# Performance work log

Measured on AMD Instinct MI355X. Metric: run time of the kernel, lower is better.

## Reference

```python
import jax, jax.numpy as jnp
import numpy as np

B, S, D_MODEL, H, D_HEAD = 4, 2048, 1024, 16, 64
SCALE = D_HEAD ** -0.5


def setup_inputs() -> dict:
    key = jax.random.key(0)
    ks = jax.random.split(key, 6)
    init = lambda k, shp: jax.random.normal(k, shp, jnp.float32) * (shp[0] ** -0.5)
    Xq = jax.random.normal(ks[0], (B, S, D_MODEL), jnp.float32)
    # pre-softmax bool mask: True = masked (fill -inf) -> causal
    mask_bef = jnp.triu(jnp.ones((S, S), dtype=bool), k=1)
    # post-softmax bool mask: True = zero out that attention weight
    mask_aft = jax.random.bernoulli(ks[1], 0.1, (S, S))
    Wq = init(ks[2], (D_MODEL, H * D_HEAD))
    Wk = init(ks[3], (D_MODEL, H * D_HEAD))
    Wv = init(ks[4], (D_MODEL, H * D_HEAD))
    Wo = init(ks[5], (H * D_HEAD, D_MODEL))
    return {"Xq": Xq, "mask_bef": mask_bef, "mask_aft": mask_aft,
            "Wq": Wq, "Wk": Wk, "Wv": Wv, "Wo": Wo}


def reference(Xq, mask_bef, mask_aft, Wq, Wk, Wv, Wo):
    # Self-attention: Xk = Xv = Xq
    def split_heads(X, W):  # [B,S,D] @ [D,H*d] -> [B,H,S,d]
        return (X @ W).reshape(B, S, H, D_HEAD).transpose(0, 2, 1, 3)

    Q = split_heads(Xq, Wq)
    K = split_heads(Xq, Wk)
    V = split_heads(Xq, Wv)
    # scores: [B,H,Sq,Sk]
    scores = jnp.einsum('bhqd,bhkd->bhqk', Q, K) * SCALE
    scores = jnp.where(mask_bef, -jnp.inf, scores)  # pre-softmax bool mask
    attn = jax.nn.softmax(scores, axis=-1)
    attn = jnp.where(mask_aft, 0.0, attn)           # post-softmax bool mask
    out = jnp.einsum('bhqk,bhkd->bhqd', attn, V)    # [B,H,S,d]
    out = out.transpose(0, 2, 1, 3).reshape(B, S, H * D_HEAD)
    return out @ Wo  # [B,S,out_dim_o]
```

## Files before the change

### kernel.cpp

```cpp
#include <hip/hip_runtime.h>
#include <hip/hip_bf16.h>


using bf16 = __hip_bfloat16;
typedef __attribute__((ext_vector_type(8))) short short8;
typedef __attribute__((ext_vector_type(4))) float floatx4;

#define kB 4
#define kS 2048
#define kDM 1024
#define kH 16
#define kDH 64
#define kHeadElems ((size_t)kB * kH * kS * kDH)
#define STR 72

__device__ __forceinline__ float bfu(unsigned short v) {
    return __uint_as_float(((unsigned)v) << 16);
}
__device__ __forceinline__ unsigned short f2bf(float f) {
    union { float f; unsigned u; } x{f};
    unsigned r = x.u + 0x7fff + ((x.u >> 16) & 1);
    return (unsigned short)(r >> 16);
}
__device__ __forceinline__ void gl_lds16(const void* g, void* l) {
    __builtin_amdgcn_global_load_lds(
        (const __attribute__((address_space(1))) unsigned int*)g,
        (__attribute__((address_space(3))) unsigned int*)l, 16, 0, 0);
}

__global__ __launch_bounds__(256)
void pack_mask(const int* __restrict__ mask_aft, unsigned long long* __restrict__ mp)
{
    const int widx = blockIdx.x * 4 + (threadIdx.x >> 6);
    const int lane = threadIdx.x & 63;
    const int q = widx >> 5, w64 = widx & 31;
    const int key = w64 * 64 + lane;
    const int m = mask_aft[(size_t)q * kS + key];
    const unsigned long long b = __ballot(m != 0 || key > q);
    if (lane == 0) mp[widx] = b;
}

__global__ __launch_bounds__(256)
void conv_x(const float* __restrict__ X, bf16* __restrict__ Xb)
{
    const size_t i = ((size_t)blockIdx.x * 256 + threadIdx.x) * 8;
    const float4 a = *(const float4*)(X + i);
    const float4 b = *(const float4*)(X + i + 4);
    union { unsigned short u[8]; uint4 v; } o;
    o.u[0] = f2bf(a.x); o.u[1] = f2bf(a.y); o.u[2] = f2bf(a.z); o.u[3] = f2bf(a.w);
    o.u[4] = f2bf(b.x); o.u[5] = f2bf(b.y); o.u[6] = f2bf(b.z); o.u[7] = f2bf(b.w);
    *(uint4*)(Xb + i) = o.v;
}

__global__ __launch_bounds__(256)
void conv_wT(const float* __restrict__ W, bf16* __restrict__ WT)
{
    __shared__ unsigned short Ls[64][STR];
    const int k0 = blockIdx.x * 64, n0 = blockIdx.y * 64;
    const int tid = threadIdx.x;
    const int r16 = tid >> 4, c4 = (tid & 15) * 4;
    #pragma unroll
    for (int it = 0; it < 4; ++it) {
        const int r = it * 16 + r16;
        const float4 v = *(const float4*)(W + (size_t)(k0 + r) * kDM + n0 + c4);
        Ls[c4 + 0][r] = f2bf(v.x); Ls[c4 + 1][r] = f2bf(v.y);
        Ls[c4 + 2][r] = f2bf(v.z); Ls[c4 + 3][r] = f2bf(v.w);
    }
    __syncthreads();
    #pragma unroll
    for (int it = 0; it < 4; ++it) {
        const int rn = it * 16 + r16;
        ushort4 u;
        u.x = Ls[rn][c4 + 0]; u.y = Ls[rn][c4 + 1];
        u.z = Ls[rn][c4 + 2]; u.w = Ls[rn][c4 + 3];
        *(ushort4*)(WT + (size_t)(n0 + rn) * kDM + k0 + c4) = u;
    }
}

__global__ __launch_bounds__(256)
void qkv_mfma(const bf16* __restrict__ A, const bf16* __restrict__ BT,
              bf16* __restrict__ ws)
{
    __shared__ __align__(16) unsigned short At[128][32];
    __shared__ __align__(16) unsigned short Bt[128][32];
    const int tid = threadIdx.x;
    const int w = tid >> 6, lane = tid & 63;
    const int quad = (tid >> 4) & 3, col = tid & 15;
    const int wm = w >> 1, wn = w & 1;
    const int n0 = blockIdx.x * 128;
    const int m0 = blockIdx.y * 128;

    const bf16* pA = A  + (size_t)(m0 + w * 32 + (lane >> 2)) * kDM + (lane & 3) * 8;
    const bf16* pB = BT + (size_t)(n0 + w * 32 + (lane >> 2)) * kDM + (lane & 3) * 8;
    unsigned short* lA = &At[w * 32][0];
    unsigned short* lB = &Bt[w * 32][0];

    floatx4 acc[4][4];
    #pragma unroll
    for (int i = 0; i < 4; ++i)
        #pragma unroll
        for (int j = 0; j < 4; ++j) acc[i][j] = (floatx4){0.f, 0.f, 0.f, 0.f};

    for (int k0 = 0; k0 < kDM; k0 += 32) {
        __syncthreads();
        gl_lds16(pA + k0, lA);
        gl_lds16(pA + k0 + 16 * kDM, lA + 16 * 32);
        gl_lds16(pB + k0, lB);
        gl_lds16(pB + k0 + 16 * kDM, lB + 16 * 32);
        __syncthreads();
        short8 aA[4], bB[4];
        #pragma unroll
        for (int i = 0; i < 4; ++i)
            aA[i] = *(const short8*)&At[wm * 64 + i * 16 + col][quad * 8];
        #pragma unroll
        for (int j = 0; j < 4; ++j)
            bB[j] = *(const short8*)&Bt[wn * 64 + j * 16 + col][quad * 8];
        #pragma unroll
        for (int i = 0; i < 4; ++i)
            #pragma unroll
            for (int j = 0; j < 4; ++j)
                acc[i][j] = __builtin_amdgcn_mfma_f32_16x16x32_bf16(aA[i], bB[j], acc[i][j], 0, 0, 0);
    }

    const int p  = n0 >> 10;
    const int nn = n0 & 1023;
    const float scl = (p == 0) ? 0.125f : 1.0f;
    bf16* Out = ws + (size_t)p * kHeadElems;
    #pragma unroll
    for (int i = 0; i < 4; ++i) {
        #pragma unroll
        for (int r = 0; r < 4; ++r) {
            const int m = m0 + wm * 64 + i * 16 + quad * 4 + r;
            const int b = m >> 11, s = m & 2047;
            #pragma unroll
            for (int j = 0; j < 4; ++j) {
                const int n = nn + wn * 64 + j * 16 + col;
                const int h = n >> 6, d = n & 63;
                Out[((size_t)(b * kH + h) * kS + s) * kDH + d] = __float2bfloat16(acc[i][j][r] * scl);
            }
        }
    }
}

__global__ __launch_bounds__(256)
void vtrans(const bf16* __restrict__ V, bf16* __restrict__ VT)
{
    const int bh = blockIdx.y;
    const int s0 = blockIdx.x * 64;
    const bf16* src = V + (size_t)bh * kS * kDH;
    bf16* dst = VT + (size_t)bh * kS * kDH;
    __shared__ unsigned short L[64][STR];
    const int tid = threadIdx.x;
    #pragma unroll
    for (int t = 0; t < 2; ++t) {
        const int idx = t * 256 + tid;
        const int r = idx >> 3, c8 = (idx & 7) * 8;
        *(uint4*)&L[r][c8] = *(const uint4*)(src + (size_t)(s0 + r) * kDH + c8);
    }
    __syncthreads();
    #pragma unroll
    for (int t = 0; t < 2; ++t) {
        const int idx = t * 256 + tid;
        const int d = idx >> 3, sc = (idx & 7) * 8;
        unsigned short tmp[8];
        #pragma unroll
        for (int e = 0; e < 8; ++e) tmp[e] = L[sc + e][d];
        *(uint4*)(dst + (size_t)d * kS + s0 + sc) = *(uint4*)tmp;
    }
}

__global__ __launch_bounds__(256)
void attn_mfma(const bf16* __restrict__ ws, const bf16* __restrict__ VT,
               const unsigned long long* __restrict__ mp,
               bf16* __restrict__ Aout)
{
    const int bh = blockIdx.y;
    const int b = bh >> 4, h = bh & 15;
    const int qtile = 31 - blockIdx.x;
    const int q0 = qtile * 64;
    const int tid = threadIdx.x;
    const int w    = tid >> 6;
    const int lane = tid & 63;
    const int quad = (tid >> 4) & 3;
    const int col  = tid & 15;

    const size_t ho = (size_t)bh * kS * kDH;
    const bf16* Qg  = ws + ho;
    const bf16* Kg  = ws + kHeadElems + ho;
    const bf16* VTg = VT + ho;

    __shared__ __align__(16) unsigned short Ks[64][64];
    __shared__ __align__(16) unsigned short Vs[64][64];
    __shared__ __align__(16) unsigned short Pw[4][16][STR];
    __shared__ unsigned long long Mw[64];

    const int qw = q0 + w * 16;
    const short8 bQ0 = *(const short8*)(Qg + (size_t)(qw + col) * kDH + quad * 8);
    const short8 bQ1 = *(const short8*)(Qg + (size_t)(qw + col) * kDH + 32 + quad * 8);

    const int swz = col & 7;
    const int sch = (lane & 7) ^ (lane >> 3);

    floatx4 Ov[4] = {{0.f,0.f,0.f,0.f},{0.f,0.f,0.f,0.f},{0.f,0.f,0.f,0.f},{0.f,0.f,0.f,0.f}};
    float lacc = 0.f;

    for (int kt = 0; kt <= qtile; ++kt) {
        __syncthreads();
        #pragma unroll
        for (int t = 0; t < 2; ++t) {
            const int rbase = (t * 4 + w) * 8;
            const int r = rbase + (lane >> 3);
            gl_lds16(Kg  + (size_t)(kt * 64 + r) * kDH + sch * 8, &Ks[rbase][0]);
            gl_lds16(VTg + (size_t)r * kS + kt * 64 + sch * 8,    &Vs[rbase][0]);
        }
        if (tid < 64) Mw[tid] = mp[(size_t)(q0 + tid) * 32 + kt];
        __syncthreads();

        floatx4 sg[4];
        #pragma unroll
        for (int g = 0; g < 4; ++g) {
            const int krow = g * 16 + col;
            const short8 aK0 = *(const short8*)&Ks[krow][(quad ^ swz) * 8];
            const short8 aK1 = *(const short8*)&Ks[krow][((4 + quad) ^ swz) * 8];
            floatx4 s = {0.f, 0.f, 0.f, 0.f};
            s = __builtin_amdgcn_mfma_f32_16x16x32_bf16(aK0, bQ0, s, 0, 0, 0);
            s = __builtin_amdgcn_mfma_f32_16x16x32_bf16(aK1, bQ1, s, 0, 0, 0);
            sg[g] = s;
        }

        const unsigned long long wr = Mw[w * 16 + col] >> (quad * 4);
        const unsigned wlo = (unsigned)wr, whi = (unsigned)(wr >> 32);
        float pv[16];
        if (kt == qtile) {
            #pragma unroll
            for (int g = 0; g < 4; ++g)
                #pragma unroll
                for (int r = 0; r < 4; ++r) {
                    const int key = kt * 64 + g * 16 + quad * 4 + r;
                    const float pe = __expf(sg[g][r]);
                    const float p = (key <= qw + col) ? pe : 0.f;
                    lacc += p;
                    const unsigned wsel = (g < 2) ? wlo : whi;
                    pv[g * 4 + r] = ((wsel >> ((g & 1) * 16 + r)) & 1u) ? 0.f : p;
                }
        } else {
            #pragma unroll
            for (int g = 0; g < 4; ++g)
                #pragma unroll
                for (int r = 0; r < 4; ++r) {
                    const float p = __expf(sg[g][r]);
                    lacc += p;
                    const unsigned wsel = (g < 2) ? wlo : whi;
                    pv[g * 4 + r] = ((wsel >> ((g & 1) * 16 + r)) & 1u) ? 0.f : p;
                }
        }

        #pragma unroll
        for (int g = 0; g < 4; ++g) {
            const unsigned b0 = __float_as_uint(pv[g * 4 + 0]) + 0x8000u;
            const unsigned b1 = __float_as_uint(pv[g * 4 + 1]) + 0x8000u;
            const unsigned b2 = __float_as_uint(pv[g * 4 + 2]) + 0x8000u;
            const unsigned b3 = __float_as_uint(pv[g * 4 + 3]) + 0x8000u;
            uint2 pk;
            pk.x = __builtin_amdgcn_perm(b1, b0, 0x07060302u);
            pk.y = __builtin_amdgcn_perm(b3, b2, 0x07060302u);
            *(uint2*)&Pw[w][col][g * 16 + quad * 4] = pk;
        }

        const short8 aP0 = *(const short8*)&Pw[w][col][quad * 8];
        const short8 aP1 = *(const short8*)&Pw[w][col][32 + quad * 8];
        #pragma unroll
        for (int dg = 0; dg < 4; ++dg) {
            const int vrow = dg * 16 + col;
            const short8 bV0 = *(const short8*)&Vs[vrow][(quad ^ swz) * 8];
            const short8 bV1 = *(const short8*)&Vs[vrow][((4 + quad) ^ swz) * 8];
            Ov[dg] = __builtin_amdgcn_mfma_f32_16x16x32_bf16(aP0, bV0, Ov[dg], 0, 0, 0);
            Ov[dg] = __builtin_amdgcn_mfma_f32_16x16x32_bf16(aP1, bV1, Ov[dg], 0, 0, 0);
        }
    }

    float l = lacc;
    l += __shfl_xor(l, 16, 64);
    l += __shfl_xor(l, 32, 64);
    const float linv = 1.f / l;
    #pragma unroll
    for (int r = 0; r < 4; ++r) {
        const float sc = __shfl(linv, quad * 4 + r, 64);
        const int q = qw + quad * 4 + r;
        bf16* orow = Aout + ((size_t)(b * kS + q)) * kDM + h * kDH;
        #pragma unroll
        for (int dg = 0; dg < 4; ++dg)
            orow[dg * 16 + col] = __float2bfloat16(Ov[dg][r] * sc);
    }
}

__global__ __launch_bounds__(256)
void out_mfma(const bf16* __restrict__ A, const bf16* __restrict__ BT,
              float* __restrict__ Out)
{
    __shared__ __align__(16) unsigned short At[128][32];
    __shared__ __align__(16) unsigned short Bt[128][32];
    const int tid = threadIdx.x;
    const int w = tid >> 6, lane = tid & 63;
    const int quad = (tid >> 4) & 3, col = tid & 15;
    const int wm = w >> 1, wn = w & 1;
    const int n0 = blockIdx.x * 128;
    const int m0 = blockIdx.y * 128;

    const bf16* pA = A  + (size_t)(m0 + w * 32 + (lane >> 2)) * kDM + (lane & 3) * 8;
    const bf16* pB = BT + (size_t)(n0 + w * 32 + (lane >> 2)) * kDM + (lane & 3) * 8;
    unsigned short* lA = &At[w * 32][0];
    unsigned short* lB = &Bt[w * 32][0];

    floatx4 acc[4][4];
    #pragma unroll
    for (int i = 0; i < 4; ++i)
        #pragma unroll
        for (int j = 0; j < 4; ++j) acc[i][j] = (floatx4){0.f, 0.f, 0.f, 0.f};

    for (int k0 = 0; k0 < kDM; k0 += 32) {
        __syncthreads();
        gl_lds16(pA + k0, lA);
        gl_lds16(pA + k0 + 16 * kDM, lA + 16 * 32);
        gl_lds16(pB + k0, lB);
        gl_lds16(pB + k0 + 16 * kDM, lB + 16 * 32);
        __syncthreads();
        short8 aA[4], bB[4];
        #pragma unroll
        for (int i = 0; i < 4; ++i)
            aA[i] = *(const short8*)&At[wm * 64 + i * 16 + col][quad * 8];
        #pragma unroll
        for (int j = 0; j < 4; ++j)
            bB[j] = *(const short8*)&Bt[wn * 64 + j * 16 + col][quad * 8];
        #pragma unroll
        for (int i = 0; i < 4; ++i)
            #pragma unroll
            for (int j = 0; j < 4; ++j)
                acc[i][j] = __builtin_amdgcn_mfma_f32_16x16x32_bf16(aA[i], bB[j], acc[i][j], 0, 0, 0);
    }

    #pragma unroll
    for (int i = 0; i < 4; ++i)
        #pragma unroll
        for (int r = 0; r < 4; ++r) {
            const int m = m0 + wm * 64 + i * 16 + quad * 4 + r;
            #pragma unroll
            for (int j = 0; j < 4; ++j)
                Out[(size_t)m * kDM + n0 + wn * 64 + j * 16 + col] = acc[i][j][r];
        }
}

extern "C" void kernel_launch(void* const* d_in, const int* in_sizes, int n_in,
                              void* d_out, int out_size, void* d_ws, size_t ws_size,
                              hipStream_t stream)
{
    const float* Xq       = (const float*)d_in[0];
    const int*   mask_aft = (const int*)d_in[2];
    const float* Wq       = (const float*)d_in[3];
    const float* Wk       = (const float*)d_in[4];
    const float* Wv       = (const float*)d_in[5];
    const float* Wo       = (const float*)d_in[6];
    float* out = (float*)d_out;

    bf16* ws   = (bf16*)d_ws;
    bf16* Xbf  = ws + 3 * kHeadElems;
    bf16* Aout = Xbf;
    bf16* WoT  = ws;

    unsigned long long* mp = (unsigned long long*)d_out;
    bf16* WcatT = (bf16*)d_out + 262144;
    bf16* VT    = (bf16*)((char*)d_out + 8u * 1024 * 1024);

    pack_mask<<<dim3(kS * 32 / 4), 256, 0, stream>>>(mask_aft, mp);
    conv_x  <<<dim3(4096), 256, 0, stream>>>(Xq, Xbf);
    conv_wT <<<dim3(16, 16), 256, 0, stream>>>(Wq, WcatT);
    conv_wT <<<dim3(16, 16), 256, 0, stream>>>(Wk, WcatT + (size_t)kDM * kDM);
    conv_wT <<<dim3(16, 16), 256, 0, stream>>>(Wv, WcatT + 2 * (size_t)kDM * kDM);
    qkv_mfma<<<dim3(24, 64), 256, 0, stream>>>(Xbf, WcatT, ws);
    vtrans  <<<dim3(32, 64), 256, 0, stream>>>(ws + 2 * kHeadElems, VT);
    attn_mfma<<<dim3(32, 64), 256, 0, stream>>>(ws, VT, mp, Aout);
    conv_wT <<<dim3(16, 16), 256, 0, stream>>>(Wo, WoT);
    out_mfma<<<dim3(8, 64), 256, 0, stream>>>(Aout, WoT, out);
}
```

Measured before the change: 350.1 us.

## Restructure attention with 128-query tiles, double-buffered K/V, exp2 and row-major QKV

The attention kernel now gives each block 128 queries (32 per wave, in two 16-row groups). K/V tiles are double-buffered so the next tile's global-to-LDS load overlaps compute, and the K and V fragments are loaded once and reused for both query groups. The softmax folds log2(e) into the Q scale so it can use exp2, and the causal check runs only on diagonal tiles. QKV is written row-major instead of head-split, and the three weight conversions are merged into one launch. Risks include higher register pressure under the 3-blocks-per-CU launch bound, fewer blocks in the grid, and strided Q/K reads.

```diff
diff --git a/kernel.cpp b/kernel.cpp
--- a/kernel.cpp
+++ b/kernel.cpp
@@ -13,10 +13,8 @@
 #define kDH 64
 #define kHeadElems ((size_t)kB * kH * kS * kDH)
 #define STR 72
-
-__device__ __forceinline__ float bfu(unsigned short v) {
-    return __uint_as_float(((unsigned)v) << 16);
-}
+#define kQScale 0.1803368801f
+
 __device__ __forceinline__ unsigned short f2bf(float f) {
     union { float f; unsigned u; } x{f};
     unsigned r = x.u + 0x7fff + ((x.u >> 16) & 1);
@@ -52,8 +50,8 @@
     *(uint4*)(Xb + i) = o.v;
 }
 
-__global__ __launch_bounds__(256)
-void conv_wT(const float* __restrict__ W, bf16* __restrict__ WT)
+__device__ __forceinline__ void conv_wT_body(const float* __restrict__ W,
+                                             bf16* __restrict__ WT)
 {
     __shared__ unsigned short Ls[64][STR];
     const int k0 = blockIdx.x * 64, n0 = blockIdx.y * 64;
@@ -75,6 +73,21 @@
         u.z = Ls[rn][c4 + 2]; u.w = Ls[rn][c4 + 3];
         *(ushort4*)(WT + (size_t)(n0 + rn) * kDM + k0 + c4) = u;
     }
+}
+
+__global__ __launch_bounds__(256)
+void conv_w3(const float* __restrict__ Wq, const float* __restrict__ Wk,
+             const float* __restrict__ Wv, bf16* __restrict__ WT)
+{
+    const int z = blockIdx.z;
+    const float* W = (z == 0) ? Wq : ((z == 1) ? Wk : Wv);
+    conv_wT_body(W, WT + (size_t)z * kDM * kDM);
+}
+
+__global__ __launch_bounds__(256)
+void conv_wT(const float* __restrict__ W, bf16* __restrict__ WT)
+{
+    conv_wT_body(W, WT);
 }
 
 __global__ __launch_bounds__(256)
@@ -122,22 +135,19 @@
                 acc[i][j] = __builtin_amdgcn_mfma_f32_16x16x32_bf16(aA[i], bB[j], acc[i][j], 0, 0, 0);
     }
 
-    const int p  = n0 >> 10;
-    const int nn = n0 & 1023;
-    const float scl = (p == 0) ? 0.125f : 1.0f;
+    const int p   = n0 >> 10;
+    const int nn0 = n0 & 1023;
+    const float scl = (p == 0) ? kQScale : 1.0f;
     bf16* Out = ws + (size_t)p * kHeadElems;
     #pragma unroll
     for (int i = 0; i < 4; ++i) {
         #pragma unroll
         for (int r = 0; r < 4; ++r) {
             const int m = m0 + wm * 64 + i * 16 + quad * 4 + r;
-            const int b = m >> 11, s = m & 2047;
-            #pragma unroll
-            for (int j = 0; j < 4; ++j) {
-                const int n = nn + wn * 64 + j * 16 + col;
-                const int h = n >> 6, d = n & 63;
-                Out[((size_t)(b * kH + h) * kS + s) * kDH + d] = __float2bfloat16(acc[i][j][r] * scl);
-            }
+            bf16* base = Out + (size_t)m * kDM + nn0 + wn * 64 + col;
+            #pragma unroll
+            for (int j = 0; j < 4; ++j)
+                base[j * 16] = __float2bfloat16(acc[i][j][r] * scl);
         }
     }
 }
@@ -146,8 +156,9 @@
 void vtrans(const bf16* __restrict__ V, bf16* __restrict__ VT)
 {
     const int bh = blockIdx.y;
+    const int b = bh >> 4, h = bh & 15;
     const int s0 = blockIdx.x * 64;
-    const bf16* src = V + (size_t)bh * kS * kDH;
+    const bf16* src = V + ((size_t)b * kS) * kDM + h * kDH;
     bf16* dst = VT + (size_t)bh * kS * kDH;
     __shared__ unsigned short L[64][STR];
     const int tid = threadIdx.x;
@@ -155,7 +166,7 @@
     for (int t = 0; t < 2; ++t) {
         const int idx = t * 256 + tid;
         const int r = idx >> 3, c8 = (idx & 7) * 8;
-        *(uint4*)&L[r][c8] = *(const uint4*)(src + (size_t)(s0 + r) * kDH + c8);
+        *(uint4*)&L[r][c8] = *(const uint4*)(src + (size_t)(s0 + r) * kDM + c8);
     }
     __syncthreads();
     #pragma unroll
@@ -169,128 +180,151 @@
     }
 }
 
-__global__ __launch_bounds__(256)
-void attn_mfma(const bf16* __restrict__ ws, const bf16* __restrict__ VT,
-               const unsigned long long* __restrict__ mp,
+__global__ __launch_bounds__(256, 3)
+void attn_mfma(const bf16* __restrict__ Qb, const bf16* __restrict__ Kb,
+               const bf16* __restrict__ VT, const unsigned long long* __restrict__ mp,
                bf16* __restrict__ Aout)
 {
     const int bh = blockIdx.y;
     const int b = bh >> 4, h = bh & 15;
-    const int qtile = 31 - blockIdx.x;
-    const int q0 = qtile * 64;
+    const int qtile = 15 - blockIdx.x;
+    const int q0 = qtile * 128;
     const int tid = threadIdx.x;
     const int w    = tid >> 6;
     const int lane = tid & 63;
     const int quad = (tid >> 4) & 3;
     const int col  = tid & 15;
 
-    const size_t ho = (size_t)bh * kS * kDH;
-    const bf16* Qg  = ws + ho;
-    const bf16* Kg  = ws + kHeadElems + ho;
-    const bf16* VTg = VT + ho;
-
-    __shared__ __align__(16) unsigned short Ks[64][64];
-    __shared__ __align__(16) unsigned short Vs[64][64];
+    const bf16* Qg  = Qb + ((size_t)b * kS) * kDM + h * kDH;
+    const bf16* Kg  = Kb + ((size_t)b * kS) * kDM + h * kDH;
+    const bf16* VTg = VT + (size_t)bh * kS * kDH;
+
+    __shared__ __align__(16) unsigned short Ks[2][64][64];
+    __shared__ __align__(16) unsigned short Vs[2][64][64];
     __shared__ __align__(16) unsigned short Pw[4][16][STR];
-    __shared__ unsigned long long Mw[64];
-
-    const int qw = q0 + w * 16;
-    const short8 bQ0 = *(const short8*)(Qg + (size_t)(qw + col) * kDH + quad * 8);
-    const short8 bQ1 = *(const short8*)(Qg + (size_t)(qw + col) * kDH + 32 + quad * 8);
+    __shared__ unsigned long long Mw[2][128];
 
     const int swz = col & 7;
     const int sch = (lane & 7) ^ (lane >> 3);
 
-    floatx4 Ov[4] = {{0.f,0.f,0.f,0.f},{0.f,0.f,0.f,0.f},{0.f,0.f,0.f,0.f},{0.f,0.f,0.f,0.f}};
-    float lacc = 0.f;
-
-    for (int kt = 0; kt <= qtile; ++kt) {
-        __syncthreads();
+    short8 bQ[2][2];
+    #pragma unroll
+    for (int qg = 0; qg < 2; ++qg) {
+        const int qr = q0 + w * 32 + qg * 16 + col;
+        bQ[qg][0] = *(const short8*)(Qg + (size_t)qr * kDM + quad * 8);
+        bQ[qg][1] = *(const short8*)(Qg + (size_t)qr * kDM + 32 + quad * 8);
+    }
+
+    floatx4 Ov[2][4];
+    #pragma unroll
+    for (int qg = 0; qg < 2; ++qg)
+        #pragma unroll
+        for (int dg = 0; dg < 4; ++dg) Ov[qg][dg] = (floatx4){0.f, 0.f, 0.f, 0.f};
+    float lacc[2] = {0.f, 0.f};
+
+    const int nkt = 2 * qtile + 2;
+
+    auto stage = [&](int kt, int buf) {
         #pragma unroll
         for (int t = 0; t < 2; ++t) {
             const int rbase = (t * 4 + w) * 8;
             const int r = rbase + (lane >> 3);
-            gl_lds16(Kg  + (size_t)(kt * 64 + r) * kDH + sch * 8, &Ks[rbase][0]);
-            gl_lds16(VTg + (size_t)r * kS + kt * 64 + sch * 8,    &Vs[rbase][0]);
-        }
-        if (tid < 64) Mw[tid] = mp[(size_t)(q0 + tid) * 32 + kt];
+            gl_lds16(Kg  + (size_t)(kt * 64 + r) * kDM + sch * 8, &Ks[buf][rbase][0]);
+            gl_lds16(VTg + (size_t)r * kS + kt * 64 + sch * 8,    &Vs[buf][rbase][0]);
+        }
+        if (tid < 128) Mw[buf][tid] = mp[(size_t)(q0 + tid) * 32 + kt];
+    };
+
+    stage(0, 0);
+
+    for (int kt = 0; kt < nkt; ++kt) {
+        const int cur = kt & 1;
         __syncthreads();
-
-        floatx4 sg[4];
+        if (kt + 1 < nkt) stage(kt + 1, cur ^ 1);
+
+        if (kt * 64 > q0 + w * 32 + 31) continue;
+
+        short8 aK[4][2];
         #pragma unroll
         for (int g = 0; g < 4; ++g) {
             const int krow = g * 16 + col;
-            const short8 aK0 = *(const short8*)&Ks[krow][(quad ^ swz) * 8];
-            const short8 aK1 = *(const short8*)&Ks[krow][((4 + quad) ^ swz) * 8];
-            floatx4 s = {0.f, 0.f, 0.f, 0.f};
-            s = __builtin_amdgcn_mfma_f32_16x16x32_bf16(aK0, bQ0, s, 0, 0, 0);
-            s = __builtin_amdgcn_mfma_f32_16x16x32_bf16(aK1, bQ1, s, 0, 0, 0);
-            sg[g] = s;
-        }
-
-        const unsigned long long wr = Mw[w * 16 + col] >> (quad * 4);
-        const unsigned wlo = (unsigned)wr, whi = (unsigned)(wr >> 32);
-        float pv[16];
-        if (kt == qtile) {
-            #pragma unroll
-            for (int g = 0; g < 4; ++g)
+            aK[g][0] = *(const short8*)&Ks[cur][krow][(quad ^ swz) * 8];
+            aK[g][1] = *(const short8*)&Ks[cur][krow][((4 + quad) ^ swz) * 8];
+        }
+        short8 bV[4][2];
+        #pragma unroll
+        for (int dg = 0; dg < 4; ++dg) {
+            const int vrow = dg * 16 + col;
+            bV[dg][0] = *(const short8*)&Vs[cur][vrow][(quad ^ swz) * 8];
+            bV[dg][1] = *(const short8*)&Vs[cur][vrow][((4 + quad) ^ swz) * 8];
+        }
+
+        #pragma unroll
+        for (int qg = 0; qg < 2; ++qg) {
+            const int qw = q0 + w * 32 + qg * 16;
+            if (kt * 64 > qw + 15) continue;
+
+            floatx4 sg[4];
+            #pragma unroll
+            for (int g = 0; g < 4; ++g) {
+                floatx4 s = {0.f, 0.f, 0.f, 0.f};
+                s = __builtin_amdgcn_mfma_f32_16x16x32_bf16(aK[g][0], bQ[qg][0], s, 0, 0, 0);
+                s = __builtin_amdgcn_mfma_f32_16x16x32_bf16(aK[g][1], bQ[qg][1], s, 0, 0, 0);
+                sg[g] = s;
+            }
+
+            const unsigned long long wr = Mw[cur][w * 32 + qg * 16 + col] >> (quad * 4);
+            const unsigned wlo = (unsigned)wr, whi = (unsigned)(wr >> 32);
+            const bool diag = (kt * 64 + 63 > qw);
+
+            #pragma unroll
+            for (int g = 0; g < 4; ++g) {
+                float pv[4];
                 #pragma unroll
                 for (int r = 0; r < 4; ++r) {
-                    const int key = kt * 64 + g * 16 + quad * 4 + r;
-                    const float pe = __expf(sg[g][r]);
-                    const float p = (key <= qw + col) ? pe : 0.f;
-                    lacc += p;
+                    float p = __builtin_amdgcn_exp2f(sg[g][r]);
+                    if (diag) {
+                        const int key = kt * 64 + g * 16 + quad * 4 + r;
+                        p = (key <= qw + col) ? p : 0.f;
+                    }
+                    lacc[qg] += p;
                     const unsigned wsel = (g < 2) ? wlo : whi;
-                    pv[g * 4 + r] = ((wsel >> ((g & 1) * 16 + r)) & 1u) ? 0.f : p;
+                    pv[r] = ((wsel >> ((g & 1) * 16 + r)) & 1u) ? 0.f : p;
                 }
-        } else {
-            #pragma unroll
-            for (int g = 0; g < 4; ++g)
-                #pragma unroll
-                for (int r = 0; r < 4; ++r) {
-                    const float p = __expf(sg[g][r]);
-                    lacc += p;
-                    const unsigned wsel = (g < 2) ? wlo : whi;
-                    pv[g * 4 + r] = ((wsel >> ((g & 1) * 16 + r)) & 1u) ? 0.f : p;
-                }
-        }
-
-        #pragma unroll
-        for (int g = 0; g < 4; ++g) {
-            const unsigned b0 = __float_as_uint(pv[g * 4 + 0]) + 0x8000u;
-            const unsigned b1 = __float_as_uint(pv[g * 4 + 1]) + 0x8000u;
-            const unsigned b2 = __float_as_uint(pv[g * 4 + 2]) + 0x8000u;
-            const unsigned b3 = __float_as_uint(pv[g * 4 + 3]) + 0x8000u;
-            uint2 pk;
-            pk.x = __builtin_amdgcn_perm(b1, b0, 0x07060302u);
-            pk.y = __builtin_amdgcn_perm(b3, b2, 0x07060302u);
-            *(uint2*)&Pw[w][col][g * 16 + quad * 4] = pk;
-        }
-
-        const short8 aP0 = *(const short8*)&Pw[w][col][quad * 8];
-        const short8 aP1 = *(const short8*)&Pw[w][col][32 + quad * 8];
-        #pragma unroll
-        for (int dg = 0; dg < 4; ++dg) {
-            const int vrow = dg * 16 + col;
-            const short8 bV0 = *(const short8*)&Vs[vrow][(quad ^ swz) * 8];
-            const short8 bV1 = *(const short8*)&Vs[vrow][((4 + quad) ^ swz) * 8];
-            Ov[dg] = __builtin_amdgcn_mfma_f32_16x16x32_bf16(aP0, bV0, Ov[dg], 0, 0, 0);
-            Ov[dg] = __builtin_amdgcn_mfma_f32_16x16x32_bf16(aP1, bV1, Ov[dg], 0, 0, 0);
-        }
-    }
-
-    float l = lacc;
-    l += __shfl_xor(l, 16, 64);
-    l += __shfl_xor(l, 32, 64);
-    const float linv = 1.f / l;
-    #pragma unroll
-    for (int r = 0; r < 4; ++r) {
-        const float sc = __shfl(linv, quad * 4 + r, 64);
-        const int q = qw + quad * 4 + r;
-        bf16* orow = Aout + ((size_t)(b * kS + q)) * kDM + h * kDH;
-        #pragma unroll
-        for (int dg = 0; dg < 4; ++dg)
-            orow[dg * 16 + col] = __float2bfloat16(Ov[dg][r] * sc);
+                const __hip_bfloat162 p01 = __float22bfloat162_rn({pv[0], pv[1]});
+                const __hip_bfloat162 p23 = __float22bfloat162_rn({pv[2], pv[3]});
+                uint2 pk;
+                pk.x = *(const unsigned*)&p01;
+                pk.y = *(const unsigned*)&p23;
+                *(uint2*)&Pw[w][col][g * 16 + quad * 4] = pk;
+            }
+
+            const short8 aP0 = *(const short8*)&Pw[w][col][quad * 8];
+            const short8 aP1 = *(const short8*)&Pw[w][col][32 + quad * 8];
+            #pragma unroll
+            for (int dg = 0; dg < 4; ++dg) {
+                Ov[qg][dg] = __builtin_amdgcn_mfma_f32_16x16x32_bf16(aP0, bV[dg][0], Ov[qg][dg], 0, 0, 0);
+                Ov[qg][dg] = __builtin_amdgcn_mfma_f32_16x16x32_bf16(aP1, bV[dg][1], Ov[qg][dg], 0, 0, 0);
+            }
+        }
+    }
+
+    #pragma unroll
+    for (int qg = 0; qg < 2; ++qg) {
+        float l = lacc[qg];
+        l += __shfl_xor(l, 16, 64);
+        l += __shfl_xor(l, 32, 64);
+        const float linv = 1.f / l;
+        const int qw = q0 + w * 32 + qg * 16;
+        #pragma unroll
+        for (int r = 0; r < 4; ++r) {
+            const float sc = __shfl(linv, quad * 4 + r, 64);
+            const int q = qw + quad * 4 + r;
+            bf16* orow = Aout + ((size_t)(b * kS + q)) * kDM + h * kDH;
+            #pragma unroll
+            for (int dg = 0; dg < 4; ++dg)
+                orow[dg * 16 + col] = __float2bfloat16(Ov[qg][dg][r] * sc);
+        }
     }
 }
 
@@ -363,22 +397,23 @@
     float* out = (float*)d_out;
 
     bf16* ws   = (bf16*)d_ws;
+    bf16* Qbuf = ws;
+    bf16* Kbuf = ws + kHeadElems;
+    bf16* Vbuf = ws + 2 * kHeadElems;
     bf16* Xbf  = ws + 3 * kHeadElems;
     bf16* Aout = Xbf;
-    bf16* WoT  = ws;
+    bf16* WoT  = Qbuf;
 
     unsigned long long* mp = (unsigned long long*)d_out;
     bf16* WcatT = (bf16*)d_out + 262144;
     bf16* VT    = (bf16*)((char*)d_out + 8u * 1024 * 1024);
 
     pack_mask<<<dim3(kS * 32 / 4), 256, 0, stream>>>(mask_aft, mp);
-    conv_x  <<<dim3(4096), 256, 0, stream>>>(Xq, Xbf);
-    conv_wT <<<dim3(16, 16), 256, 0, stream>>>(Wq, WcatT);
-    conv_wT <<<dim3(16, 16), 256, 0, stream>>>(Wk, WcatT + (size_t)kDM * kDM);
-    conv_wT <<<dim3(16, 16), 256, 0, stream>>>(Wv, WcatT + 2 * (size_t)kDM * kDM);
-    qkv_mfma<<<dim3(24, 64), 256, 0, stream>>>(Xbf, WcatT, ws);
-    vtrans  <<<dim3(32, 64), 256, 0, stream>>>(ws + 2 * kHeadElems, VT);
-    attn_mfma<<<dim3(32, 64), 256, 0, stream>>>(ws, VT, mp, Aout);
-    conv_wT <<<dim3(16, 16), 256, 0, stream>>>(Wo, WoT);
-    out_mfma<<<dim3(8, 64), 256, 0, stream>>>(Aout, WoT, out);
-}
+    conv_x   <<<dim3(4096), 256, 0, stream>>>(Xq, Xbf);
+    conv_w3  <<<dim3(16, 16, 3), 256, 0, stream>>>(Wq, Wk, Wv, WcatT);
+    qkv_mfma <<<dim3(24, 64), 256, 0, stream>>>(Xbf, WcatT, ws);
+    vtrans   <<<dim3(32, 64), 256, 0, stream>>>(Vbuf, VT);
+    attn_mfma<<<dim3(16, 64), 256, 0, stream>>>(Qbuf, Kbuf, VT, mp, Aout);
+    conv_wT  <<<dim3(16, 16), 256, 0, stream>>>(Wo, WoT);
+    out_mfma <<<dim3(8, 64), 256, 0, stream>>>(Aout, WoT, out);
+}
```

After: 394.9 us. +12.8%, slower.
